# Optimization experiments

Hardware: AMD Instinct MI355X
Metric: run time of the kernel (lower is better)

Reference implementation:

```python
import jax, jax.numpy as jnp
import numpy as np

LGRAD = 27.8   # gradient scale (module _lgrad)
LCOL = 10.0    # color scale   (module _lcol)
MAXLVL = 4     # merge levels  (module _maxlvl)
FINAL_TH = 0.0 # merge threshold (module _final_th)


def _grad_mag(feat):
    # per-pixel gradient magnitude, averaged over channels -> [B,H,W]
    gx = jnp.pad(feat[..., :, 1:] - feat[..., :, :-1], ((0, 0), (0, 0), (0, 0), (0, 1)))
    gy = jnp.pad(feat[..., 1:, :] - feat[..., :-1, :], ((0, 0), (0, 0), (0, 1), (0, 0)))
    return jnp.sqrt(gx * gx + gy * gy + 1e-12).mean(axis=1)


def _edges(H, W):
    # directed 4-connectivity edge list over the pixel grid (static, numpy)
    idx = np.arange(H * W).reshape(H, W)
    hu, hv = idx[:, :-1].ravel(), idx[:, 1:].ravel()
    vu, vv = idx[:-1, :].ravel(), idx[1:, :].ravel()
    src = np.concatenate([hu, hv, vu, vv]).astype(np.int32)
    dst = np.concatenate([hv, hu, vv, vu]).astype(np.int32)
    return jnp.asarray(src), jnp.asarray(dst)


def _merge_level(labels, pix, gmag, src, dst, N):
    # labels [N] int32 pixel->region, pix [N,3], gmag [N]
    ones = jnp.ones_like(gmag)
    cnt = jax.ops.segment_sum(ones, labels, num_segments=N)
    csum = jax.ops.segment_sum(pix, labels, num_segments=N)
    gsum = jax.ops.segment_sum(gmag, labels, num_segments=N)
    safe = jnp.maximum(cnt, 1.0)
    mcol = csum / safe[:, None]      # region mean color [N,3]
    mg = gsum / safe                 # region mean gradient [N]

    la, lb = labels[src], labels[dst]
    valid = la != lb
    dc = jnp.sqrt(jnp.sum((mcol[la] - mcol[lb]) ** 2, axis=-1) + 1e-12)
    ge = 0.5 * (mg[la] + mg[lb])
    sim = jnp.exp(-(dc / LCOL + ge / LGRAD))     # in (0,1], higher = more similar
    sim = jnp.where(valid, sim, -1.0)

    best = jax.ops.segment_max(sim, la, num_segments=N)     # best-neighbor similarity
    cand = jnp.where(valid & (sim == best[la]), lb, jnp.int32(N))
    bn = jax.ops.segment_min(cand, la, num_segments=N)      # deterministic best neighbor id

    r = jnp.arange(N, dtype=jnp.int32)
    bnc = jnp.clip(bn, 0, N - 1)
    mutual = (bn < N) & (bnc[bnc] == r) & (best > FINAL_TH)  # mutual-best, cycle-free pairs
    parent = jnp.where(mutual, jnp.minimum(r, bnc), r)
    return parent[labels]


def _tokenize(feat):
    B, C, H, W = feat.shape
    N = H * W
    gmag = _grad_mag(feat).reshape(B, N)
    pix = feat.reshape(B, C, N).transpose(0, 2, 1)            # [B,N,3]
    src, dst = _edges(H, W)
    labels = jnp.broadcast_to(jnp.arange(N, dtype=jnp.int32), (B, N))

    step = jax.vmap(lambda l, p, g: _merge_level(l, p, g, src, dst, N))
    for _ in range(MAXLVL):
        labels = step(labels, pix, gmag)

    def mean_map(l, p):
        cnt = jax.ops.segment_sum(jnp.ones((N,), p.dtype), l, num_segments=N)
        cs = jax.ops.segment_sum(p, l, num_segments=N)
        return (cs / jnp.maximum(cnt, 1.0)[:, None])[l]

    colmap = jax.vmap(mean_map)(labels, pix)                  # [B,N,3] region-mean colors
    colmap = colmap.transpose(0, 2, 1).reshape(B, C, H, W)
    return labels.reshape(B, H, W), colmap


def setup_inputs() -> dict:
    key = jax.random.key(0)
    feat = jax.random.uniform(key, (8, 3, 512, 512), dtype=jnp.float32) * 255.0
    return {"feat": feat}


def reference(feat):
    return _tokenize(feat)
```

## Files before the change

### kernel.cpp

```cpp
#include <hip/hip_runtime.h>
#include <math.h>

#define WW 512
#define HH 512
#define NPIX (WW*HH)
#define NSH 18
#define NXCD 8

typedef unsigned long long u64;
typedef unsigned int u32;
typedef unsigned short u16;

__device__ __forceinline__ u64 umax64(u64 a, u64 b) { return a > b ? a : b; }

__device__ __forceinline__ int swz_idx() {
  int g = gridDim.x;
  int b = (int)blockIdx.x;
  int nb2 = (b & (NXCD - 1)) * (g >> 3) + (b >> 3);
  return nb2 * 256 + (int)threadIdx.x;
}

__device__ __forceinline__ void tile_coords(int& bb, int& x0, int& y0) {
  int g = gridDim.x;
  int b = (int)blockIdx.x;
  int t = (b & (NXCD - 1)) * (g >> 3) + (b >> 3);
  bb = t >> 10;
  int rem = t & 1023;
  y0 = (rem >> 4) << 3;
  x0 = (rem & 15) << 5;
}

__device__ __forceinline__ float d_colg(const float* __restrict__ fb, int p, int pw, int ph,
                                        float col[3]) {
  float s = 0.f;
#pragma unroll
  for (int c = 0; c < 3; ++c) {
    const float* fc = fb + (size_t)c * NPIX;
    float v = fc[p];
    col[c] = v;
    float gx = (pw < WW - 1) ? __fsub_rn(fc[p + 1], v) : 0.f;
    float gy = (ph < HH - 1) ? __fsub_rn(fc[p + WW], v) : 0.f;
    float g = __fsqrt_rn(__fadd_rn(__fadd_rn(__fmul_rn(gx, gx), __fmul_rn(gy, gy)), 1e-12f));
    s = __fadd_rn(s, g);
  }
  return __fdiv_rn(s, 3.0f);
}

__device__ __forceinline__ u64 d_simbits(float4 a, float4 b) {
  float d0 = __fsub_rn(a.x, b.x);
  float d1 = __fsub_rn(a.y, b.y);
  float d2 = __fsub_rn(a.z, b.z);
  float ss = __fadd_rn(__fadd_rn(__fmul_rn(d0, d0), __fmul_rn(d1, d1)), __fmul_rn(d2, d2));
  float dc = __fsqrt_rn(__fadd_rn(ss, 1e-12f));
  float ge = __fmul_rn(0.5f, __fadd_rn(a.w, b.w));
  float t = __fadd_rn(__fdiv_rn(dc, 10.0f), __fdiv_rn(ge, 27.8f));
  float sim = (float)exp(-(double)t);
  return ((u64)__float_as_uint(sim)) << 32;
}

__global__ __launch_bounds__(256) void k_prep0edge(const float* __restrict__ feat,
                                                   int* __restrict__ labels,
                                                   int* __restrict__ cnt,
                                                   float4* __restrict__ pix4,
                                                   float4* __restrict__ mcol4,
                                                   u64* __restrict__ bnkey) {
  __shared__ float4 scolg[340];
  __shared__ u64 skey[256];
  int bb, x0, y0;
  tile_coords(bb, x0, y0);
  const float* fb = feat + (size_t)bb * 3 * NPIX;
  int tid = (int)threadIdx.x;
  skey[tid] = 0;
  for (int c = tid; c < 340; c += 256) {
    int cx = (c % 34) - 1, cy = (c / 34) - 1;
    int x = x0 + cx, y = y0 + cy;
    if (x >= 0 && x < WW && y >= 0 && y < HH) {
      float col[3];
      float g = d_colg(fb, y * WW + x, x, y, col);
      scolg[c] = make_float4(col[0], col[1], col[2], g);
    }
  }
  __syncthreads();
  int tx = tid & 31, ty = tid >> 5;
  int x = x0 + tx, y = y0 + ty;
  int n = y * WW + x;
  int idx = (bb << NSH) + n;
  int cell = (ty + 1) * 34 + (tx + 1);
  float4 ca = scolg[cell];
  labels[idx] = n;
  cnt[idx] = 1;
  pix4[idx] = ca;
  mcol4[idx] = ca;
  u64 key = 0;
  if (x < WW - 1) {
    u64 s = d_simbits(ca, scolg[cell + 1]);
    key = umax64(key, s | (u32)(NPIX - (n + 1)));
    if (tx < 31) atomicMax(&skey[tid + 1], s | (u32)(NPIX - n));
  }
  if (tx == 0 && x > 0) {
    u64 s = d_simbits(ca, scolg[cell - 1]);
    key = umax64(key, s | (u32)(NPIX - (n - 1)));
  }
  if (y < HH - 1) {
    u64 s = d_simbits(ca, scolg[cell + 34]);
    key = umax64(key, s | (u32)(NPIX - (n + WW)));
    if (ty < 7) atomicMax(&skey[tid + 32], s | (u32)(NPIX - n));
  }
  if (ty == 0 && y > 0) {
    u64 s = d_simbits(ca, scolg[cell - 34]);
    key = umax64(key, s | (u32)(NPIX - (n - WW)));
  }
  __syncthreads();
  bnkey[idx] = umax64(key, skey[tid]);
}

__global__ __launch_bounds__(256) void k_edge(const int* __restrict__ labels,
                                              const float4* __restrict__ mcol4,
                                              u64* __restrict__ bnkey, int lvl) {
  __shared__ int sla[256];
  __shared__ float4 sma[256];
  __shared__ u64 skey[256];
  int bb, x0, y0;
  tile_coords(bb, x0, y0);
  int tid = (int)threadIdx.x;
  int tx = tid & 31, ty = tid >> 5;
  int x = x0 + tx, y = y0 + ty;
  int n = y * WW + x;
  int base = bb << NSH;
  int idx = base + n;
  int la = labels[idx];
  float4 ma = mcol4[base + la];
  sla[tid] = la;
  sma[tid] = ma;
  skey[tid] = 0;
  __syncthreads();
  u64 key = 0;
  if (x < WW - 1) {
    if (tx < 31) {
      int lb = sla[tid + 1];
      if (lb != la) {
        u64 s = d_simbits(ma, sma[tid + 1]);
        key = umax64(key, s | (u32)(NPIX - lb));
        atomicMax(&skey[tid + 1], s | (u32)(NPIX - la));
      }
    } else {
      int lb = labels[idx + 1];
      if (lb != la) key = umax64(key, d_simbits(ma, mcol4[base + lb]) | (u32)(NPIX - lb));
    }
  }
  if (tx == 0 && x > 0) {
    int lb = labels[idx - 1];
    if (lb != la) key = umax64(key, d_simbits(ma, mcol4[base + lb]) | (u32)(NPIX - lb));
  }
  if (y < HH - 1) {
    if (ty < 7) {
      int lb = sla[tid + 32];
      if (lb != la) {
        u64 s = d_simbits(ma, sma[tid + 32]);
        key = umax64(key, s | (u32)(NPIX - lb));
        atomicMax(&skey[tid + 32], s | (u32)(NPIX - la));
      }
    } else {
      int lb = labels[idx + WW];
      if (lb != la) key = umax64(key, d_simbits(ma, mcol4[base + lb]) | (u32)(NPIX - lb));
    }
  }
  if (ty == 0 && y > 0) {
    int lb = labels[idx - WW];
    if (lb != la) key = umax64(key, d_simbits(ma, mcol4[base + lb]) | (u32)(NPIX - lb));
  }
  __syncthreads();
  u64 val = umax64(key, skey[tid]);
  if (val) atomicMax(&bnkey[base + la], ((u64)lvl << 62) | val);
}

template<bool LVL0, bool LAST>
__global__ __launch_bounds__(256) void k_scanpairs(int* __restrict__ labels,
                                                   int* __restrict__ cnt,
                                                   u16* __restrict__ mem,
                                                   const u64* __restrict__ bnkey,
                                                   const float4* __restrict__ pix4,
                                                   float4* __restrict__ mcol4,
                                                   int total, int lvl) {
  __shared__ u64 swl[256];
  __shared__ int scnt;
  if (threadIdx.x == 0) scnt = 0;
  __syncthreads();

  int idx = swz_idx();
  bool pred = false;
  u64 e = 0;
  if (idx < total) {
    int n = idx & (NPIX - 1);
    int base = idx - n;
    u64 K = bnkey[idx];
    bool valid = LVL0 ? true : ((int)(K >> 62) == lvl);
    if (valid) {
      int v = NPIX - (int)(K & 0xffffffffu);
      if (v < NPIX && n < v) {
        u64 Kv = bnkey[base + v];
        bool pv = LVL0 ? true : ((int)(Kv >> 62) == lvl);
        if (pv && NPIX - (int)(Kv & 0xffffffffu) == n) {
          pred = true;
          e = ((u64)(u32)idx << 32) | (u32)v;
        }
      }
    }
  }

  u64 mask = __ballot(pred);
  int lane = (int)(threadIdx.x & 63);
  int wb0 = 0;
  if (lane == 0 && mask) wb0 = atomicAdd(&scnt, __popcll(mask));
  int wb = __shfl(wb0, 0);
  if (pred) {
    int pos = wb + __popcll(mask & ((1ull << lane) - 1ull));
    swl[pos] = e;
  }
  __syncthreads();
  int m = scnt;
  if ((int)threadIdx.x >= m) return;

  e = swl[threadIdx.x];
  int idx2 = (int)(e >> 32);
  int v = (int)(e & 0xffffffffu);
  int n = idx2 & (NPIX - 1);
  int base = idx2 - n;
  float s0, s1, s2, sg;
  int k;
  u16* mo = mem + ((size_t)idx2 << 4);
  if (LVL0) {
    k = 2;
    float4 pa = pix4[idx2];
    float4 pb = pix4[base + v];
    s0 = __fadd_rn(__fadd_rn(0.f, pa.x), pb.x);
    s1 = __fadd_rn(__fadd_rn(0.f, pa.y), pb.y);
    s2 = __fadd_rn(__fadd_rn(0.f, pa.z), pb.z);
    sg = __fadd_rn(__fadd_rn(0.f, pa.w), pb.w);
    mo[0] = 0; mo[1] = (u16)(v - n);
    labels[idx2] = n;
    labels[base + v] = n;
  } else {
    int c = cnt[idx2];
    int cb = cnt[base + v];
    const u16* ma = mem + ((size_t)idx2 << 4);
    const u16* mb = mem + ((size_t)(base + v) << 4);
    k = c + cb;
    s0 = s1 = s2 = sg = 0.f;
    int i = 0, j = 0;
    while (i < c || j < cb) {
      int av = (i < c) ? ((c == 1) ? n : n + (int)ma[i]) : 0x7fffffff;
      int bv = (j < cb) ? ((cb == 1) ? v : v + (int)mb[j]) : 0x7fffffff;
      int x;
      if (av < bv) { x = av; ++i; } else { x = bv; ++j; }
      float4 p = pix4[base + x];
      s0 = __fadd_rn(s0, p.x);
      s1 = __fadd_rn(s1, p.y);
      s2 = __fadd_rn(s2, p.z);
      sg = __fadd_rn(sg, p.w);
      if (!LAST) labels[base + x] = n;
    }
    if (!LAST) {
      int i2 = c - 1, j2 = cb - 1;
      for (int t2 = k - 1; t2 >= 0; --t2) {
        int av = (i2 >= 0) ? ((c == 1) ? n : n + (int)ma[i2]) : (int)0x80000000;
        int bv = (j2 >= 0) ? ((cb == 1) ? v : v + (int)mb[j2]) : (int)0x80000000;
        int x;
        if (av > bv) { x = av; --i2; } else { x = bv; --j2; }
        mo[t2] = (u16)(x - n);
      }
    }
  }
  float safe = (float)k;
  mcol4[idx2] = make_float4(__fdiv_rn(s0, safe), __fdiv_rn(s1, safe),
                            __fdiv_rn(s2, safe), __fdiv_rn(sg, safe));
  if (LAST) {
    cnt[base + v] = -n;
  } else {
    cnt[idx2] = k;
    cnt[base + v] = 0;
  }
}

__global__ __launch_bounds__(256) void k_out(const int* __restrict__ labels,
                                             const int* __restrict__ cnt,
                                             const float4* __restrict__ mcol4,
                                             float* __restrict__ out, int total,
                                             int b0, int Btot) {
  int idx = swz_idx();
  if (idx >= total) return;
  int b = idx >> NSH;
  int n = idx & (NPIX - 1);
  int base = b << NSH;
  int l = labels[idx];
  int c2 = cnt[base + l];
  if (c2 <= 0) l = -c2;
  out[(size_t)(b0 + b) * NPIX + n] = (float)l;
  size_t cb = (size_t)Btot * NPIX;
  float4 m = mcol4[base + l];
  out[cb + ((size_t)(b0 + b) * 3 + 0) * NPIX + n] = m.x;
  out[cb + ((size_t)(b0 + b) * 3 + 1) * NPIX + n] = m.y;
  out[cb + ((size_t)(b0 + b) * 3 + 2) * NPIX + n] = m.z;
}

extern "C" void kernel_launch(void* const* d_in, const int* in_sizes, int n_in,
                              void* d_out, int out_size, void* d_ws, size_t ws_size,
                              hipStream_t stream) {
  const float* feat = (const float*)d_in[0];
  float* out = (float*)d_out;
  int Btot = in_sizes[0] / (3 * NPIX);

  const size_t perB = (size_t)NPIX * 80;
  int nbmax = (int)(ws_size / perB);
  if (nbmax < 1) nbmax = 1;
  if (nbmax > Btot) nbmax = Btot;

  for (int b0 = 0; b0 < Btot; b0 += nbmax) {
    int nb = (Btot - b0 < nbmax) ? (Btot - b0) : nbmax;
    size_t cn = (size_t)nb << NSH;
    char* p = (char*)d_ws;
    float4* mcol4 = (float4*)p; p += cn * 16;
    float4* pix4 = (float4*)p;  p += cn * 16;
    u64* key = (u64*)p;         p += cn * 8;
    int* labels = (int*)p;      p += cn * 4;
    int* cnt = (int*)p;         p += cn * 4;
    u16* mem = (u16*)p;

    const float* fchunk = feat + (size_t)b0 * 3 * NPIX;
    int total = (int)cn;
    int grid = total >> 8;

    k_prep0edge<<<grid, 256, 0, stream>>>(fchunk, labels, cnt, pix4, mcol4, key);
    k_scanpairs<true, false><<<grid, 256, 0, stream>>>(labels, cnt, mem, key,
                                                       pix4, mcol4, total, 0);
    k_edge<<<grid, 256, 0, stream>>>(labels, mcol4, key, 1);
    k_scanpairs<false, false><<<grid, 256, 0, stream>>>(labels, cnt, mem, key,
                                                        pix4, mcol4, total, 1);
    k_edge<<<grid, 256, 0, stream>>>(labels, mcol4, key, 2);
    k_scanpairs<false, false><<<grid, 256, 0, stream>>>(labels, cnt, mem, key,
                                                        pix4, mcol4, total, 2);
    k_edge<<<grid, 256, 0, stream>>>(labels, mcol4, key, 3);
    k_scanpairs<false, true><<<grid, 256, 0, stream>>>(labels, cnt, mem, key,
                                                       pix4, mcol4, total, 3);
    k_out<<<grid, 256, 0, stream>>>(labels, cnt, mcol4, out, total, b0, Btot);
  }
}
```

Measured before the change: 292.2 us.

## Fuse level-0 pair merge into prep kernel and process two rows per thread in edge

The level-0 mutual-best-neighbor detection and pair merge move into the prep kernel. A 2-pixel halo lets each pixel recompute its neighbor's best key locally, which removes one scanpairs launch and the global bnkey round trip. k_edge now covers 32x16 tiles with each thread handling two rows, it reuses the right-edge similarity when the down neighbor has the same label, and it merges the atomics when both pixels share a label. A memset of the key buffer replaces the level-0 key initialization, so the level tag in the top bits still validates. The costs are extra halo loads, recomputation of neighbor keys, and a larger shared-memory footprint.

```diff
diff --git a/kernel.cpp b/kernel.cpp
--- a/kernel.cpp
+++ b/kernel.cpp
@@ -27,6 +27,16 @@
   bb = t >> 10;
   int rem = t & 1023;
   y0 = (rem >> 4) << 3;
+  x0 = (rem & 15) << 5;
+}
+
+__device__ __forceinline__ void tile_coords_e(int& bb, int& x0, int& y0) {
+  int g = gridDim.x;
+  int b = (int)blockIdx.x;
+  int t = (b & (NXCD - 1)) * (g >> 3) + (b >> 3);
+  bb = t >> 9;
+  int rem = t & 511;
+  y0 = (rem >> 4) << 4;
   x0 = (rem & 15) << 5;
 }
 
@@ -58,21 +68,21 @@
   return ((u64)__float_as_uint(sim)) << 32;
 }
 
-__global__ __launch_bounds__(256) void k_prep0edge(const float* __restrict__ feat,
-                                                   int* __restrict__ labels,
-                                                   int* __restrict__ cnt,
-                                                   float4* __restrict__ pix4,
-                                                   float4* __restrict__ mcol4,
-                                                   u64* __restrict__ bnkey) {
-  __shared__ float4 scolg[340];
+__global__ __launch_bounds__(256) void k_prep0(const float* __restrict__ feat,
+                                               int* __restrict__ labels,
+                                               int* __restrict__ cnt,
+                                               float4* __restrict__ pix4,
+                                               float4* __restrict__ mcol4,
+                                               u16* __restrict__ mem) {
+  __shared__ float4 scolg[432];
   __shared__ u64 skey[256];
   int bb, x0, y0;
   tile_coords(bb, x0, y0);
   const float* fb = feat + (size_t)bb * 3 * NPIX;
   int tid = (int)threadIdx.x;
   skey[tid] = 0;
-  for (int c = tid; c < 340; c += 256) {
-    int cx = (c % 34) - 1, cy = (c / 34) - 1;
+  for (int c = tid; c < 432; c += 256) {
+    int cx = (c % 36) - 2, cy = (c / 36) - 2;
     int x = x0 + cx, y = y0 + cy;
     if (x >= 0 && x < WW && y >= 0 && y < HH) {
       float col[3];
@@ -85,96 +95,146 @@
   int x = x0 + tx, y = y0 + ty;
   int n = y * WW + x;
   int idx = (bb << NSH) + n;
-  int cell = (ty + 1) * 34 + (tx + 1);
-  float4 ca = scolg[cell];
-  labels[idx] = n;
-  cnt[idx] = 1;
+  int cc = (ty + 2) * 36 + (tx + 2);
+  float4 ca = scolg[cc];
   pix4[idx] = ca;
-  mcol4[idx] = ca;
   u64 key = 0;
   if (x < WW - 1) {
-    u64 s = d_simbits(ca, scolg[cell + 1]);
+    u64 s = d_simbits(ca, scolg[cc + 1]);
     key = umax64(key, s | (u32)(NPIX - (n + 1)));
     if (tx < 31) atomicMax(&skey[tid + 1], s | (u32)(NPIX - n));
   }
-  if (tx == 0 && x > 0) {
-    u64 s = d_simbits(ca, scolg[cell - 1]);
-    key = umax64(key, s | (u32)(NPIX - (n - 1)));
-  }
+  if (tx == 0 && x > 0)
+    key = umax64(key, d_simbits(ca, scolg[cc - 1]) | (u32)(NPIX - (n - 1)));
   if (y < HH - 1) {
-    u64 s = d_simbits(ca, scolg[cell + 34]);
+    u64 s = d_simbits(ca, scolg[cc + 36]);
     key = umax64(key, s | (u32)(NPIX - (n + WW)));
     if (ty < 7) atomicMax(&skey[tid + 32], s | (u32)(NPIX - n));
   }
-  if (ty == 0 && y > 0) {
-    u64 s = d_simbits(ca, scolg[cell - 34]);
-    key = umax64(key, s | (u32)(NPIX - (n - WW)));
-  }
-  __syncthreads();
-  bnkey[idx] = umax64(key, skey[tid]);
+  if (ty == 0 && y > 0)
+    key = umax64(key, d_simbits(ca, scolg[cc - 36]) | (u32)(NPIX - (n - WW)));
+  __syncthreads();
+  key = umax64(key, skey[tid]);
+  skey[tid] = key;
+  __syncthreads();
+
+  int v = NPIX - (int)(key & 0xffffffffu);
+  int vx = v & (WW - 1), vy = v >> 9;
+  u64 kv;
+  if (vx >= x0 && vx < x0 + 32 && vy >= y0 && vy < y0 + 8) {
+    kv = skey[(vy - y0) * 32 + (vx - x0)];
+  } else {
+    int vc = (vy - y0 + 2) * 36 + (vx - x0 + 2);
+    float4 cv = scolg[vc];
+    kv = 0;
+    if (vx < WW - 1) kv = umax64(kv, d_simbits(cv, scolg[vc + 1]) | (u32)(NPIX - (v + 1)));
+    if (vx > 0)      kv = umax64(kv, d_simbits(cv, scolg[vc - 1]) | (u32)(NPIX - (v - 1)));
+    if (vy < HH - 1) kv = umax64(kv, d_simbits(cv, scolg[vc + 36]) | (u32)(NPIX - (v + WW)));
+    if (vy > 0)      kv = umax64(kv, d_simbits(cv, scolg[vc - 36]) | (u32)(NPIX - (v - WW)));
+  }
+  bool mutual = (NPIX - (int)(kv & 0xffffffffu)) == n;
+  if (mutual) {
+    if (n < v) {
+      float4 pb = scolg[(vy - y0 + 2) * 36 + (vx - x0 + 2)];
+      float s0 = __fadd_rn(__fadd_rn(0.f, ca.x), pb.x);
+      float s1 = __fadd_rn(__fadd_rn(0.f, ca.y), pb.y);
+      float s2 = __fadd_rn(__fadd_rn(0.f, ca.z), pb.z);
+      float sg = __fadd_rn(__fadd_rn(0.f, ca.w), pb.w);
+      mcol4[idx] = make_float4(__fdiv_rn(s0, 2.0f), __fdiv_rn(s1, 2.0f),
+                               __fdiv_rn(s2, 2.0f), __fdiv_rn(sg, 2.0f));
+      labels[idx] = n;
+      cnt[idx] = 2;
+      u16* mo = mem + ((size_t)idx << 4);
+      mo[0] = 0; mo[1] = (u16)(v - n);
+    } else {
+      labels[idx] = v;
+      cnt[idx] = 0;
+      mcol4[idx] = ca;
+    }
+  } else {
+    labels[idx] = n;
+    cnt[idx] = 1;
+    mcol4[idx] = ca;
+  }
 }
 
 __global__ __launch_bounds__(256) void k_edge(const int* __restrict__ labels,
                                               const float4* __restrict__ mcol4,
                                               u64* __restrict__ bnkey, int lvl) {
-  __shared__ int sla[256];
-  __shared__ float4 sma[256];
-  __shared__ u64 skey[256];
+  __shared__ int sla[512];
+  __shared__ float4 sma[512];
+  __shared__ u64 skey[512];
   int bb, x0, y0;
-  tile_coords(bb, x0, y0);
+  tile_coords_e(bb, x0, y0);
   int tid = (int)threadIdx.x;
-  int tx = tid & 31, ty = tid >> 5;
-  int x = x0 + tx, y = y0 + ty;
-  int n = y * WW + x;
   int base = bb << NSH;
-  int idx = base + n;
-  int la = labels[idx];
-  float4 ma = mcol4[base + la];
-  sla[tid] = la;
-  sma[tid] = ma;
-  skey[tid] = 0;
-  __syncthreads();
-  u64 key = 0;
-  if (x < WW - 1) {
-    if (tx < 31) {
-      int lb = sla[tid + 1];
-      if (lb != la) {
-        u64 s = d_simbits(ma, sma[tid + 1]);
-        key = umax64(key, s | (u32)(NPIX - lb));
-        atomicMax(&skey[tid + 1], s | (u32)(NPIX - la));
+  int n0 = (y0 + (tid >> 5)) * WW + x0 + (tid & 31);
+  int n1 = n0 + 8 * WW;
+  int l0 = labels[base + n0];
+  int l1 = labels[base + n1];
+  float4 m0 = mcol4[base + l0];
+  float4 m1 = mcol4[base + l1];
+  sla[tid] = l0; sla[tid + 256] = l1;
+  sma[tid] = m0; sma[tid + 256] = m1;
+  skey[tid] = 0; skey[tid + 256] = 0;
+  __syncthreads();
+  auto edges = [&](int s, int n, int l, float4 m) -> u64 {
+    int tx = s & 31, ty = s >> 5;
+    int x = x0 + tx, y = y0 + ty;
+    u64 key = 0;
+    int lbR = -1; u64 sR = 0;
+    if (x < WW - 1) {
+      if (tx < 31) {
+        int lb = sla[s + 1];
+        if (lb != l) {
+          sR = d_simbits(m, sma[s + 1]); lbR = lb;
+          key = umax64(key, sR | (u32)(NPIX - lb));
+          atomicMax(&skey[s + 1], sR | (u32)(NPIX - l));
+        }
+      } else {
+        int lb = labels[base + n + 1];
+        if (lb != l) key = umax64(key, d_simbits(m, mcol4[base + lb]) | (u32)(NPIX - lb));
       }
-    } else {
-      int lb = labels[idx + 1];
-      if (lb != la) key = umax64(key, d_simbits(ma, mcol4[base + lb]) | (u32)(NPIX - lb));
-    }
-  }
-  if (tx == 0 && x > 0) {
-    int lb = labels[idx - 1];
-    if (lb != la) key = umax64(key, d_simbits(ma, mcol4[base + lb]) | (u32)(NPIX - lb));
-  }
-  if (y < HH - 1) {
-    if (ty < 7) {
-      int lb = sla[tid + 32];
-      if (lb != la) {
-        u64 s = d_simbits(ma, sma[tid + 32]);
-        key = umax64(key, s | (u32)(NPIX - lb));
-        atomicMax(&skey[tid + 32], s | (u32)(NPIX - la));
+    }
+    if (tx == 0 && x > 0) {
+      int lb = labels[base + n - 1];
+      if (lb != l) key = umax64(key, d_simbits(m, mcol4[base + lb]) | (u32)(NPIX - lb));
+    }
+    if (y < HH - 1) {
+      if (ty < 15) {
+        int lb = sla[s + 32];
+        if (lb != l) {
+          u64 sD = (lb == lbR) ? sR : d_simbits(m, sma[s + 32]);
+          key = umax64(key, sD | (u32)(NPIX - lb));
+          atomicMax(&skey[s + 32], sD | (u32)(NPIX - l));
+        }
+      } else {
+        int lb = labels[base + n + WW];
+        if (lb != l) key = umax64(key, d_simbits(m, mcol4[base + lb]) | (u32)(NPIX - lb));
       }
-    } else {
-      int lb = labels[idx + WW];
-      if (lb != la) key = umax64(key, d_simbits(ma, mcol4[base + lb]) | (u32)(NPIX - lb));
-    }
-  }
-  if (ty == 0 && y > 0) {
-    int lb = labels[idx - WW];
-    if (lb != la) key = umax64(key, d_simbits(ma, mcol4[base + lb]) | (u32)(NPIX - lb));
-  }
-  __syncthreads();
-  u64 val = umax64(key, skey[tid]);
-  if (val) atomicMax(&bnkey[base + la], ((u64)lvl << 62) | val);
-}
-
-template<bool LVL0, bool LAST>
+    }
+    if (ty == 0 && y > 0) {
+      int lb = labels[base + n - WW];
+      if (lb != l) key = umax64(key, d_simbits(m, mcol4[base + lb]) | (u32)(NPIX - lb));
+    }
+    return key;
+  };
+  u64 k0 = edges(tid, n0, l0, m0);
+  u64 k1 = edges(tid + 256, n1, l1, m1);
+  __syncthreads();
+  k0 = umax64(k0, skey[tid]);
+  k1 = umax64(k1, skey[tid + 256]);
+  u64 tg = (u64)lvl << 62;
+  if (l0 == l1) {
+    u64 kk = umax64(k0, k1);
+    if (kk) atomicMax(&bnkey[base + l0], tg | kk);
+  } else {
+    if (k0) atomicMax(&bnkey[base + l0], tg | k0);
+    if (k1) atomicMax(&bnkey[base + l1], tg | k1);
+  }
+}
+
+template<bool LAST>
 __global__ __launch_bounds__(256) void k_scanpairs(int* __restrict__ labels,
                                                    int* __restrict__ cnt,
                                                    u16* __restrict__ mem,
@@ -194,13 +254,11 @@
     int n = idx & (NPIX - 1);
     int base = idx - n;
     u64 K = bnkey[idx];
-    bool valid = LVL0 ? true : ((int)(K >> 62) == lvl);
-    if (valid) {
+    if ((int)(K >> 62) == lvl) {
       int v = NPIX - (int)(K & 0xffffffffu);
       if (v < NPIX && n < v) {
         u64 Kv = bnkey[base + v];
-        bool pv = LVL0 ? true : ((int)(Kv >> 62) == lvl);
-        if (pv && NPIX - (int)(Kv & 0xffffffffu) == n) {
+        if ((int)(Kv >> 62) == lvl && NPIX - (int)(Kv & 0xffffffffu) == n) {
           pred = true;
           e = ((u64)(u32)idx << 32) | (u32)v;
         }
@@ -226,49 +284,34 @@
   int v = (int)(e & 0xffffffffu);
   int n = idx2 & (NPIX - 1);
   int base = idx2 - n;
-  float s0, s1, s2, sg;
-  int k;
-  u16* mo = mem + ((size_t)idx2 << 4);
-  if (LVL0) {
-    k = 2;
-    float4 pa = pix4[idx2];
-    float4 pb = pix4[base + v];
-    s0 = __fadd_rn(__fadd_rn(0.f, pa.x), pb.x);
-    s1 = __fadd_rn(__fadd_rn(0.f, pa.y), pb.y);
-    s2 = __fadd_rn(__fadd_rn(0.f, pa.z), pb.z);
-    sg = __fadd_rn(__fadd_rn(0.f, pa.w), pb.w);
-    mo[0] = 0; mo[1] = (u16)(v - n);
-    labels[idx2] = n;
-    labels[base + v] = n;
-  } else {
-    int c = cnt[idx2];
-    int cb = cnt[base + v];
-    const u16* ma = mem + ((size_t)idx2 << 4);
-    const u16* mb = mem + ((size_t)(base + v) << 4);
-    k = c + cb;
-    s0 = s1 = s2 = sg = 0.f;
-    int i = 0, j = 0;
-    while (i < c || j < cb) {
-      int av = (i < c) ? ((c == 1) ? n : n + (int)ma[i]) : 0x7fffffff;
-      int bv = (j < cb) ? ((cb == 1) ? v : v + (int)mb[j]) : 0x7fffffff;
+  int c = cnt[idx2];
+  int cb = cnt[base + v];
+  const u16* ma = mem + ((size_t)idx2 << 4);
+  const u16* mb = mem + ((size_t)(base + v) << 4);
+  int k = c + cb;
+  float s0 = 0.f, s1 = 0.f, s2 = 0.f, sg = 0.f;
+  int i = 0, j = 0;
+  while (i < c || j < cb) {
+    int av = (i < c) ? ((c == 1) ? n : n + (int)ma[i]) : 0x7fffffff;
+    int bv = (j < cb) ? ((cb == 1) ? v : v + (int)mb[j]) : 0x7fffffff;
+    int x;
+    if (av < bv) { x = av; ++i; } else { x = bv; ++j; }
+    float4 p = pix4[base + x];
+    s0 = __fadd_rn(s0, p.x);
+    s1 = __fadd_rn(s1, p.y);
+    s2 = __fadd_rn(s2, p.z);
+    sg = __fadd_rn(sg, p.w);
+    if (!LAST) labels[base + x] = n;
+  }
+  if (!LAST) {
+    u16* mo = mem + ((size_t)idx2 << 4);
+    int i2 = c - 1, j2 = cb - 1;
+    for (int t2 = k - 1; t2 >= 0; --t2) {
+      int av = (i2 >= 0) ? ((c == 1) ? n : n + (int)ma[i2]) : (int)0x80000000;
+      int bv = (j2 >= 0) ? ((cb == 1) ? v : v + (int)mb[j2]) : (int)0x80000000;
       int x;
-      if (av < bv) { x = av; ++i; } else { x = bv; ++j; }
-      float4 p = pix4[base + x];
-      s0 = __fadd_rn(s0, p.x);
-      s1 = __fadd_rn(s1, p.y);
-      s2 = __fadd_rn(s2, p.z);
-      sg = __fadd_rn(sg, p.w);
-      if (!LAST) labels[base + x] = n;
-    }
-    if (!LAST) {
-      int i2 = c - 1, j2 = cb - 1;
-      for (int t2 = k - 1; t2 >= 0; --t2) {
-        int av = (i2 >= 0) ? ((c == 1) ? n : n + (int)ma[i2]) : (int)0x80000000;
-        int bv = (j2 >= 0) ? ((cb == 1) ? v : v + (int)mb[j2]) : (int)0x80000000;
-        int x;
-        if (av > bv) { x = av; --i2; } else { x = bv; --j2; }
-        mo[t2] = (u16)(x - n);
-      }
+      if (av > bv) { x = av; --i2; } else { x = bv; --j2; }
+      mo[t2] = (u16)(x - n);
     }
   }
   float safe = (float)k;
@@ -329,19 +372,20 @@
     const float* fchunk = feat + (size_t)b0 * 3 * NPIX;
     int total = (int)cn;
     int grid = total >> 8;
-
-    k_prep0edge<<<grid, 256, 0, stream>>>(fchunk, labels, cnt, pix4, mcol4, key);
-    k_scanpairs<true, false><<<grid, 256, 0, stream>>>(labels, cnt, mem, key,
-                                                       pix4, mcol4, total, 0);
-    k_edge<<<grid, 256, 0, stream>>>(labels, mcol4, key, 1);
-    k_scanpairs<false, false><<<grid, 256, 0, stream>>>(labels, cnt, mem, key,
-                                                        pix4, mcol4, total, 1);
-    k_edge<<<grid, 256, 0, stream>>>(labels, mcol4, key, 2);
-    k_scanpairs<false, false><<<grid, 256, 0, stream>>>(labels, cnt, mem, key,
-                                                        pix4, mcol4, total, 2);
-    k_edge<<<grid, 256, 0, stream>>>(labels, mcol4, key, 3);
-    k_scanpairs<false, true><<<grid, 256, 0, stream>>>(labels, cnt, mem, key,
-                                                       pix4, mcol4, total, 3);
+    int gride = total >> 9;
+
+    hipMemsetAsync(key, 0, cn * 8, stream);
+
+    k_prep0<<<grid, 256, 0, stream>>>(fchunk, labels, cnt, pix4, mcol4, mem);
+    k_edge<<<gride, 256, 0, stream>>>(labels, mcol4, key, 1);
+    k_scanpairs<false><<<grid, 256, 0, stream>>>(labels, cnt, mem, key,
+                                                 pix4, mcol4, total, 1);
+    k_edge<<<gride, 256, 0, stream>>>(labels, mcol4, key, 2);
+    k_scanpairs<false><<<grid, 256, 0, stream>>>(labels, cnt, mem, key,
+                                                 pix4, mcol4, total, 2);
+    k_edge<<<gride, 256, 0, stream>>>(labels, mcol4, key, 3);
+    k_scanpairs<true><<<grid, 256, 0, stream>>>(labels, cnt, mem, key,
+                                                pix4, mcol4, total, 3);
     k_out<<<grid, 256, 0, stream>>>(labels, cnt, mcol4, out, total, b0, Btot);
   }
 }
```

Measured after the change: 303.2 us. 3.8% more time.
